# Performance work log

Measured on AMD Instinct MI355X. Metric: run time of the kernel, lower is better.

The kernel has to match this reference:

```python
import jax, jax.numpy as jnp
import numpy as np

TAU_MEM = 20.0
TAU_SYN = 5.0
ALPHA_MEM = float(np.exp(-1.0 / TAU_MEM))
ALPHA_SYN = float(np.exp(-1.0 / TAU_SYN))
CONNECTIVITY = 0.1
SPECTRAL_RADIUS = 0.9


def setup_inputs() -> dict:
    key = jax.random.key(0)
    k1, k2, k3, k4 = jax.random.split(key, 4)
    B, D, N = 2048, 256, 512
    rates = jax.random.normal(k1, (B, D), dtype=jnp.float32)
    input_weight = jax.random.normal(k2, (N, D), dtype=jnp.float32) * 0.1
    W = jax.random.normal(k3, (N, N), dtype=jnp.float32)
    mask = (jax.random.uniform(k4, (N, N)) < CONNECTIVITY).astype(jnp.float32)
    W = W * mask
    # mirror torch init: scale by spectral_radius / max eigvalsh
    max_eig = jnp.linalg.eigvalsh(W)[-1]
    W = W * (SPECTRAL_RADIUS / max_eig)
    return {
        "rates": rates,
        "input_weight": input_weight,
        "reservoir_weight": W,
        "v_mem": jnp.zeros((B, N), dtype=jnp.float32),
        "current": jnp.zeros((B, N), dtype=jnp.float32),
        "n_steps": 64,
    }


def reference(rates, input_weight, reservoir_weight, v_mem, current, n_steps):
    dtype = rates.dtype
    # input current is identical every step in the original loop -> hoist it
    input_current = rates @ input_weight.T  # (B, N)

    def step(carry, _):
        v, c, spike_sum = carry
        rec = (c > 0).astype(dtype) @ reservoir_weight  # (B, N)
        c = ALPHA_SYN * c + (1.0 - ALPHA_SYN) * (input_current + rec)
        v = ALPHA_MEM * v + (1.0 - ALPHA_MEM) * c
        spike_sum = spike_sum + (v > 0).astype(dtype)
        return (v, c, spike_sum), None

    (v, c, spike_sum), _ = jax.lax.scan(
        step, (v_mem, current, jnp.zeros_like(v_mem)), None, length=n_steps
    )
    readout = spike_sum / n_steps  # == stack(spikes).mean(dim=1)
    return readout, (v, c)
```

## Files before the change

kernel.cpp:

```cpp
#include <hip/hip_runtime.h>
#include <stdint.h>


#define N_NEU 512
#define B_ROWS 2048
#define D_IN 256
#define R_PB 8
#define NBLK (B_ROWS / R_PB)

#define WS_PERM    0
#define WS_RANK    2048
#define WS_CNT     4096
#define WS_CNTW    8192
#define WS_IBASE   8256
#define WS_WBASE   8320
#define WS_IDX     16384
#define WS_WT      81920

#define SPK_OFF(k)  ((k) << 4)
#define SPK_BUF     8192

#define H16_ONE 0x3C00u

__global__ __launch_bounds__(256) void lsm_count(
    const float* __restrict__ W, uint32_t* __restrict__ ws)
{
    int t  = threadIdx.x;
    int k0 = blockIdx.x * 4;
    int c0 = 0, c1 = 0;
    #pragma unroll
    for (int kk = 0; kk < 4; ++kk) {
        const float* row = W + (size_t)(k0 + kk) * N_NEU;
        c0 += (row[t]       != 0.0f) ? 1 : 0;
        c1 += (row[t + 256] != 0.0f) ? 1 : 0;
    }
    if (c0) atomicAdd(&ws[(WS_CNT >> 2) + t],       (uint32_t)c0);
    if (c1) atomicAdd(&ws[(WS_CNT >> 2) + t + 256], (uint32_t)c1);
}

__global__ __launch_bounds__(512) void lsm_sort(uint32_t* __restrict__ ws)
{
    __shared__ int hist[N_NEU + 1];
    __shared__ int csort[N_NEU];
    __shared__ int gcw[8];

    int t = threadIdx.x;
    int creal = (int)ws[(WS_CNT >> 2) + t];
    for (int i = t; i < N_NEU + 1; i += 512) hist[i] = 0;
    __syncthreads();
    atomicAdd(&hist[creal], 1);
    __syncthreads();
    if (t == 0) {
        int acc = 0;
        for (int v = 0; v <= N_NEU; ++v) { int h = hist[v]; hist[v] = acc; acc += h; }
    }
    __syncthreads();
    int rank = atomicAdd(&hist[creal], 1);
    ws[(WS_PERM >> 2) + rank] = (uint32_t)t;
    ws[(WS_RANK >> 2) + t]    = (uint32_t)rank;
    csort[rank] = creal;
    __syncthreads();
    if (t < 8) {
        int cw = csort[t * 64 + 63];
        cw = (cw + 7) & ~7;
        gcw[t] = cw;
        ws[(WS_CNTW >> 2) + t] = (uint32_t)cw;
    }
    __syncthreads();
    if (t == 0) {
        int ai = 0, aw = 0;
        for (int g = 0; g < 8; ++g) {
            ws[(WS_IBASE >> 2) + g] = (uint32_t)ai;
            ws[(WS_WBASE >> 2) + g] = (uint32_t)aw;
            ai += gcw[g] * 64 * 2;
            aw += gcw[g] * 64 * 4;
        }
    }
    __syncthreads();
    int wg = rank >> 6, ls = rank & 63;
    int cw = gcw[wg];
    uint32_t ib = ws[(WS_IBASE >> 2) + wg];
    uint32_t wb = ws[(WS_WBASE >> 2) + wg];
    char* base = (char*)ws;
    for (int j = creal; j < cw; ++j) {
        *(unsigned short*)(base + WS_IDX + ib + (j >> 3) * 1024 + ls * 16 + (j & 7) * 2) = 0;
        *(float*)(base + WS_WT + wb + (j >> 3) * 2048 + ls * 32 + (j & 7) * 4) = 0.0f;
    }
}

__global__ __launch_bounds__(64) void lsm_fill(
    const float* __restrict__ W, uint32_t* __restrict__ ws)
{
    int c    = blockIdx.x;
    int lane = threadIdx.x;
    char* base = (char*)ws;
    uint32_t rank = ws[(WS_RANK >> 2) + c];
    int wg = (int)(rank >> 6), ls = (int)(rank & 63);
    uint32_t ib = ws[(WS_IBASE >> 2) + wg];
    uint32_t wb = ws[(WS_WBASE >> 2) + wg];
    int rot = ls & 7;

    __shared__ int bcnt[8];
    __shared__ int bcur[8];
    if (lane < 8) bcnt[lane] = 0;
    __syncthreads();

    for (int k = lane; k < N_NEU; k += 64) {
        float wv = W[(size_t)k * N_NEU + c];
        if (wv != 0.0f) {
            int r = ((k & 7) - rot) & 7;
            atomicAdd(&bcnt[r], 1);
        }
    }
    __syncthreads();
    if (lane == 0) {
        int acc = 0;
        for (int r = 0; r < 8; ++r) { bcur[r] = acc; acc += bcnt[r]; }
    }
    __syncthreads();

    for (int k = lane; k < N_NEU; k += 64) {
        float wv = W[(size_t)k * N_NEU + c];
        if (wv != 0.0f) {
            int r = ((k & 7) - rot) & 7;
            int j = atomicAdd(&bcur[r], 1);
            *(unsigned short*)(base + WS_IDX + ib + (j >> 3) * 1024 + ls * 16 + (j & 7) * 2)
                = (unsigned short)SPK_OFF(k);
            *(float*)(base + WS_WT + wb + (j >> 3) * 2048 + ls * 32 + (j & 7) * 4) = wv;
        }
    }
}

#define GATH(P, X, B) \
    P##0 = *(const uint4*)((B) + ((X).x & 0xffffu)); \
    P##1 = *(const uint4*)((B) + ((X).x >> 16));     \
    P##2 = *(const uint4*)((B) + ((X).y & 0xffffu)); \
    P##3 = *(const uint4*)((B) + ((X).y >> 16));     \
    P##4 = *(const uint4*)((B) + ((X).z & 0xffffu)); \
    P##5 = *(const uint4*)((B) + ((X).z >> 16));     \
    P##6 = *(const uint4*)((B) + ((X).w & 0xffffu)); \
    P##7 = *(const uint4*)((B) + ((X).w >> 16));

#define FMIX_LO(ACC, WV, S) \
    asm("v_fma_mix_f32 %0, %1, %2, %0 op_sel:[0,0,0] op_sel_hi:[0,1,0]" \
        : "+v"(ACC) : "v"(WV), "v"(S));
#define FMIX_HI(ACC, WV, S) \
    asm("v_fma_mix_f32 %0, %1, %2, %0 op_sel:[0,1,0] op_sel_hi:[0,1,0]" \
        : "+v"(ACC) : "v"(WV), "v"(S));

#define C1(S, WV) \
    FMIX_LO(rec0, WV, (S).x) FMIX_HI(rec1, WV, (S).x) \
    FMIX_LO(rec2, WV, (S).y) FMIX_HI(rec3, WV, (S).y) \
    FMIX_LO(rec4, WV, (S).z) FMIX_HI(rec5, WV, (S).z) \
    FMIX_LO(rec6, WV, (S).w) FMIX_HI(rec7, WV, (S).w)

#define CONS(P, WA, WB) \
    C1(P##0, (WA).x) C1(P##1, (WA).y) C1(P##2, (WA).z) C1(P##3, (WA).w) \
    C1(P##4, (WB).x) C1(P##5, (WB).y) C1(P##6, (WB).z) C1(P##7, (WB).w)

#define LDW(WA, WB, K) \
    WA = ((const float4*)(wp0 + (K) * 2048))[0]; \
    WB = ((const float4*)(wp0 + (K) * 2048))[1];

__global__ __launch_bounds__(512, 1)
void lsm_main(
    const float* __restrict__ rates, const float* __restrict__ inW,
    const float* __restrict__ vin,   const float* __restrict__ cin,
    const int* __restrict__ nsteps_p,
    const uint32_t* __restrict__ ws, float* __restrict__ out)
{
    __shared__ __align__(16) unsigned char smem[2 * SPK_BUF + 16384];
    float* stg = (float*)(smem + 2 * SPK_BUF);
    float* rl  = stg;

    int q    = threadIdx.x;
    int blk  = blockIdx.x;
    int r0   = blk * R_PB;
    int w    = q >> 6;
    int lane = q & 63;
    int wg   = (w < 4) ? w : (11 - w);
    int n    = (int)ws[(WS_PERM >> 2) + wg * 64 + lane];
    int cw   = (int)ws[(WS_CNTW >> 2) + wg];
    int nit  = cw >> 3;
    const char* ip0 = (const char*)ws + WS_IDX + ws[(WS_IBASE >> 2) + wg]
                    + lane * 16;
    const char* wp0 = (const char*)ws + WS_WT  + ws[(WS_WBASE >> 2) + wg]
                    + lane * 32;
    int spk_n = SPK_OFF(n);

    float c0v[R_PB], v0v[R_PB];
    #pragma unroll
    for (int r = 0; r < R_PB; ++r)
        stg[r * N_NEU + q] = cin[(size_t)(r0 + r) * N_NEU + q];
    __syncthreads();
    #pragma unroll
    for (int r = 0; r < R_PB; ++r) c0v[r] = stg[r * N_NEU + n];
    __syncthreads();
    #pragma unroll
    for (int r = 0; r < R_PB; ++r)
        stg[r * N_NEU + q] = vin[(size_t)(r0 + r) * N_NEU + q];
    __syncthreads();
    #pragma unroll
    for (int r = 0; r < R_PB; ++r) v0v[r] = stg[r * N_NEU + n];
    __syncthreads();

    ((float4*)rl)[q] = ((const float4*)(rates + (size_t)r0 * D_IN))[q];
    __syncthreads();

    float I[R_PB] = {0.f, 0.f, 0.f, 0.f, 0.f, 0.f, 0.f, 0.f};
    {
        const float4* wrow = (const float4*)(inW + (size_t)n * D_IN);
        for (int d4 = 0; d4 < D_IN / 4; ++d4) {
            float4 wv = wrow[d4];
            #pragma unroll
            for (int r = 0; r < R_PB; ++r) {
                const float* rr = rl + r * D_IN + d4 * 4;
                I[r] += wv.x * rr[0] + wv.y * rr[1] + wv.z * rr[2] + wv.w * rr[3];
            }
        }
    }

    uint4 sini = make_uint4(0u, 0u, 0u, 0u);
    #pragma unroll
    for (int r = 0; r < R_PB; ++r) {
        unsigned hb = (c0v[r] > 0.f) ? H16_ONE : 0u;
        unsigned sh = (r & 1) ? 16 : 0;
        if (r < 2)      sini.x |= hb << sh;
        else if (r < 4) sini.y |= hb << sh;
        else if (r < 6) sini.z |= hb << sh;
        else            sini.w |= hb << sh;
    }
    *(uint4*)(smem + spk_n) = sini;

    unsigned ssx = 0u, ssy = 0u;

    uint4 xr0, xr1, xr2, xr3, xr4, xr5, xr6, xr7, xr8, xr9, xr10, xr11;
    const uint4 xz = make_uint4(0u, 0u, 0u, 0u);
    xr0  =              *(const uint4*)(ip0);
    xr1  = (1  < nit) ? *(const uint4*)(ip0 + 1024)  : xz;
    xr2  = (2  < nit) ? *(const uint4*)(ip0 + 2048)  : xz;
    xr3  = (3  < nit) ? *(const uint4*)(ip0 + 3072)  : xz;
    xr4  = (4  < nit) ? *(const uint4*)(ip0 + 4096)  : xz;
    xr5  = (5  < nit) ? *(const uint4*)(ip0 + 5120)  : xz;
    xr6  = (6  < nit) ? *(const uint4*)(ip0 + 6144)  : xz;
    xr7  = (7  < nit) ? *(const uint4*)(ip0 + 7168)  : xz;
    xr8  = (8  < nit) ? *(const uint4*)(ip0 + 8192)  : xz;
    xr9  = (9  < nit) ? *(const uint4*)(ip0 + 9216)  : xz;
    xr10 = (10 < nit) ? *(const uint4*)(ip0 + 10240) : xz;
    xr11 = (11 < nit) ? *(const uint4*)(ip0 + 11264) : xz;

    const float AS   = (float)0.8187307530779818;
    const float OMAS = (float)(1.0 - 0.8187307530779818);
    const float AM   = (float)0.9512294245007140;
    const float OMAM = (float)(1.0 - 0.9512294245007140);

    int T = nsteps_p[0];
    __syncthreads();

    #pragma unroll 1
    for (int t = 0; t < T; ++t) {
        const unsigned char* sb = smem + ((t & 1) ? SPK_BUF : 0);
        unsigned char*       db = smem + ((t & 1) ? 0 : SPK_BUF);

        float rec0 = 0.f, rec1 = 0.f, rec2 = 0.f, rec3 = 0.f;
        float rec4 = 0.f, rec5 = 0.f, rec6 = 0.f, rec7 = 0.f;
        uint4 a0, a1, a2, a3, a4, a5, a6, a7;
        uint4 b0, b1, b2, b3, b4, b5, b6, b7;
        float4 waA, wbA, waB, wbB;

        LDW(waA, wbA, 0)
        GATH(a, xr0, sb)
        if (1 < nit)  { LDW(waB, wbB, 1)  GATH(b, xr1, sb)  }
        CONS(a, waA, wbA)
        if (1 < nit)  {
            if (2 < nit)  { LDW(waA, wbA, 2)  GATH(a, xr2, sb)  }
            CONS(b, waB, wbB)
        }
        if (2 < nit)  {
            if (3 < nit)  { LDW(waB, wbB, 3)  GATH(b, xr3, sb)  }
            CONS(a, waA, wbA)
        }
        if (3 < nit)  {
            if (4 < nit)  { LDW(waA, wbA, 4)  GATH(a, xr4, sb)  }
            CONS(b, waB, wbB)
        }
        if (4 < nit)  {
            if (5 < nit)  { LDW(waB, wbB, 5)  GATH(b, xr5, sb)  }
            CONS(a, waA, wbA)
        }
        if (5 < nit)  {
            if (6 < nit)  { LDW(waA, wbA, 6)  GATH(a, xr6, sb)  }
            CONS(b, waB, wbB)
        }
        if (6 < nit)  {
            if (7 < nit)  { LDW(waB, wbB, 7)  GATH(b, xr7, sb)  }
            CONS(a, waA, wbA)
        }
        if (7 < nit)  {
            if (8 < nit)  { LDW(waA, wbA, 8)  GATH(a, xr8, sb)  }
            CONS(b, waB, wbB)
        }
        if (8 < nit)  {
            if (9 < nit)  { LDW(waB, wbB, 9)  GATH(b, xr9, sb)  }
            CONS(a, waA, wbA)
        }
        if (9 < nit)  {
            if (10 < nit) { LDW(waA, wbA, 10) GATH(a, xr10, sb) }
            CONS(b, waB, wbB)
        }
        if (10 < nit) {
            if (11 < nit) { LDW(waB, wbB, 11) GATH(b, xr11, sb) }
            CONS(a, waA, wbA)
        }
        if (11 < nit) {
            CONS(b, waB, wbB)
        }

        uint4 ns = make_uint4(0u, 0u, 0u, 0u);
        unsigned vbx = 0u, vby = 0u;
        {
            float rca[R_PB] = {rec0, rec1, rec2, rec3, rec4, rec5, rec6, rec7};
            #pragma unroll
            for (int r = 0; r < R_PB; ++r) {
                c0v[r] = AS * c0v[r] + OMAS * (I[r] + rca[r]);
                v0v[r] = AM * v0v[r] + OMAM * c0v[r];
                unsigned hb = (c0v[r] > 0.f) ? H16_ONE : 0u;
                unsigned vb = (v0v[r] > 0.f) ? 1u : 0u;
                unsigned sh = (r & 1) ? 16 : 0;
                if (r < 2)      ns.x |= hb << sh;
                else if (r < 4) ns.y |= hb << sh;
                else if (r < 6) ns.z |= hb << sh;
                else            ns.w |= hb << sh;
                if (r < 4) vbx |= vb << (r * 8);
                else       vby |= vb << ((r - 4) * 8);
            }
        }
        ssx += vbx;
        ssy += vby;
        *(uint4*)(db + spk_n) = ns;
        __syncthreads();
    }

    float invT = 1.0f / (float)T;
    size_t BN = (size_t)B_ROWS * N_NEU;

    #pragma unroll
    for (int r = 0; r < R_PB; ++r) {
        unsigned cnt = (r < 4) ? ((ssx >> (r * 8)) & 0xffu)
                               : ((ssy >> ((r - 4) * 8)) & 0xffu);
        stg[r * N_NEU + n] = (float)cnt * invT;
    }
    __syncthreads();
    #pragma unroll
    for (int r = 0; r < R_PB; ++r)
        out[(size_t)(r0 + r) * N_NEU + q] = stg[r * N_NEU + q];
    __syncthreads();

    #pragma unroll
    for (int r = 0; r < R_PB; ++r) stg[r * N_NEU + n] = v0v[r];
    __syncthreads();
    #pragma unroll
    for (int r = 0; r < R_PB; ++r)
        out[BN + (size_t)(r0 + r) * N_NEU + q] = stg[r * N_NEU + q];
    __syncthreads();

    #pragma unroll
    for (int r = 0; r < R_PB; ++r) stg[r * N_NEU + n] = c0v[r];
    __syncthreads();
    #pragma unroll
    for (int r = 0; r < R_PB; ++r)
        out[2 * BN + (size_t)(r0 + r) * N_NEU + q] = stg[r * N_NEU + q];
}

extern "C" void kernel_launch(void* const* d_in, const int* in_sizes, int n_in,
                              void* d_out, int out_size, void* d_ws, size_t ws_size,
                              hipStream_t stream)
{
    const float* rates = (const float*)d_in[0];
    const float* inW   = (const float*)d_in[1];
    const float* W     = (const float*)d_in[2];
    const float* vin   = (const float*)d_in[3];
    const float* cin   = (const float*)d_in[4];
    const int*   nst   = (const int*)d_in[5];
    uint32_t* ws = (uint32_t*)d_ws;
    float* out = (float*)d_out;
    (void)in_sizes; (void)n_in; (void)out_size; (void)ws_size;

    hipMemsetAsync((char*)d_ws + WS_CNT, 0, 2048, stream);

    lsm_count<<<128, 256, 0, stream>>>(W, ws);
    lsm_sort<<<1, 512, 0, stream>>>(ws);
    lsm_fill<<<N_NEU, 64, 0, stream>>>(W, ws);
    lsm_main<<<NBLK, 512, 0, stream>>>(rates, inW, vin, cin, nst, ws, out);
}
```

Before: 327.3 us.

## Fuse sparse-weight preprocessing and main loop into one cooperative kernel

Replaces the memset plus three preprocessing kernels (count, sort, fill) and the main kernel with a single cooperative launch that uses grid-wide syncs between phases. Each of the 256 blocks handles two rows or columns of the reservoir matrix during counting and filling, and block 0 does the sort. The goal is to remove several kernel launch gaps. In exchange it adds four grid barriers and requires all 256 blocks to be co-resident. The extra shared memory might also affect occupancy or whether the launch succeeds.

```diff
diff --git a/kernel.cpp b/kernel.cpp
--- a/kernel.cpp
+++ b/kernel.cpp
@@ -1,5 +1,8 @@
 #include <hip/hip_runtime.h>
+#include <hip/hip_cooperative_groups.h>
 #include <stdint.h>
+
+namespace cg = cooperative_groups;
 
 
 #define N_NEU 512
@@ -21,115 +24,6 @@
 #define SPK_BUF     8192
 
 #define H16_ONE 0x3C00u
-
-__global__ __launch_bounds__(256) void lsm_count(
-    const float* __restrict__ W, uint32_t* __restrict__ ws)
-{
-    int t  = threadIdx.x;
-    int k0 = blockIdx.x * 4;
-    int c0 = 0, c1 = 0;
-    #pragma unroll
-    for (int kk = 0; kk < 4; ++kk) {
-        const float* row = W + (size_t)(k0 + kk) * N_NEU;
-        c0 += (row[t]       != 0.0f) ? 1 : 0;
-        c1 += (row[t + 256] != 0.0f) ? 1 : 0;
-    }
-    if (c0) atomicAdd(&ws[(WS_CNT >> 2) + t],       (uint32_t)c0);
-    if (c1) atomicAdd(&ws[(WS_CNT >> 2) + t + 256], (uint32_t)c1);
-}
-
-__global__ __launch_bounds__(512) void lsm_sort(uint32_t* __restrict__ ws)
-{
-    __shared__ int hist[N_NEU + 1];
-    __shared__ int csort[N_NEU];
-    __shared__ int gcw[8];
-
-    int t = threadIdx.x;
-    int creal = (int)ws[(WS_CNT >> 2) + t];
-    for (int i = t; i < N_NEU + 1; i += 512) hist[i] = 0;
-    __syncthreads();
-    atomicAdd(&hist[creal], 1);
-    __syncthreads();
-    if (t == 0) {
-        int acc = 0;
-        for (int v = 0; v <= N_NEU; ++v) { int h = hist[v]; hist[v] = acc; acc += h; }
-    }
-    __syncthreads();
-    int rank = atomicAdd(&hist[creal], 1);
-    ws[(WS_PERM >> 2) + rank] = (uint32_t)t;
-    ws[(WS_RANK >> 2) + t]    = (uint32_t)rank;
-    csort[rank] = creal;
-    __syncthreads();
-    if (t < 8) {
-        int cw = csort[t * 64 + 63];
-        cw = (cw + 7) & ~7;
-        gcw[t] = cw;
-        ws[(WS_CNTW >> 2) + t] = (uint32_t)cw;
-    }
-    __syncthreads();
-    if (t == 0) {
-        int ai = 0, aw = 0;
-        for (int g = 0; g < 8; ++g) {
-            ws[(WS_IBASE >> 2) + g] = (uint32_t)ai;
-            ws[(WS_WBASE >> 2) + g] = (uint32_t)aw;
-            ai += gcw[g] * 64 * 2;
-            aw += gcw[g] * 64 * 4;
-        }
-    }
-    __syncthreads();
-    int wg = rank >> 6, ls = rank & 63;
-    int cw = gcw[wg];
-    uint32_t ib = ws[(WS_IBASE >> 2) + wg];
-    uint32_t wb = ws[(WS_WBASE >> 2) + wg];
-    char* base = (char*)ws;
-    for (int j = creal; j < cw; ++j) {
-        *(unsigned short*)(base + WS_IDX + ib + (j >> 3) * 1024 + ls * 16 + (j & 7) * 2) = 0;
-        *(float*)(base + WS_WT + wb + (j >> 3) * 2048 + ls * 32 + (j & 7) * 4) = 0.0f;
-    }
-}
-
-__global__ __launch_bounds__(64) void lsm_fill(
-    const float* __restrict__ W, uint32_t* __restrict__ ws)
-{
-    int c    = blockIdx.x;
-    int lane = threadIdx.x;
-    char* base = (char*)ws;
-    uint32_t rank = ws[(WS_RANK >> 2) + c];
-    int wg = (int)(rank >> 6), ls = (int)(rank & 63);
-    uint32_t ib = ws[(WS_IBASE >> 2) + wg];
-    uint32_t wb = ws[(WS_WBASE >> 2) + wg];
-    int rot = ls & 7;
-
-    __shared__ int bcnt[8];
-    __shared__ int bcur[8];
-    if (lane < 8) bcnt[lane] = 0;
-    __syncthreads();
-
-    for (int k = lane; k < N_NEU; k += 64) {
-        float wv = W[(size_t)k * N_NEU + c];
-        if (wv != 0.0f) {
-            int r = ((k & 7) - rot) & 7;
-            atomicAdd(&bcnt[r], 1);
-        }
-    }
-    __syncthreads();
-    if (lane == 0) {
-        int acc = 0;
-        for (int r = 0; r < 8; ++r) { bcur[r] = acc; acc += bcnt[r]; }
-    }
-    __syncthreads();
-
-    for (int k = lane; k < N_NEU; k += 64) {
-        float wv = W[(size_t)k * N_NEU + c];
-        if (wv != 0.0f) {
-            int r = ((k & 7) - rot) & 7;
-            int j = atomicAdd(&bcur[r], 1);
-            *(unsigned short*)(base + WS_IDX + ib + (j >> 3) * 1024 + ls * 16 + (j & 7) * 2)
-                = (unsigned short)SPK_OFF(k);
-            *(float*)(base + WS_WT + wb + (j >> 3) * 2048 + ls * 32 + (j & 7) * 4) = wv;
-        }
-    }
-}
 
 #define GATH(P, X, B) \
     P##0 = *(const uint4*)((B) + ((X).x & 0xffffu)); \
@@ -163,18 +57,129 @@
     WB = ((const float4*)(wp0 + (K) * 2048))[1];
 
 __global__ __launch_bounds__(512, 1)
-void lsm_main(
+void lsm_all(
     const float* __restrict__ rates, const float* __restrict__ inW,
+    const float* __restrict__ W,
     const float* __restrict__ vin,   const float* __restrict__ cin,
     const int* __restrict__ nsteps_p,
-    const uint32_t* __restrict__ ws, float* __restrict__ out)
+    uint32_t* __restrict__ ws, float* __restrict__ out)
 {
+    cg::grid_group grid = cg::this_grid();
+
     __shared__ __align__(16) unsigned char smem[2 * SPK_BUF + 16384];
+    __shared__ int hist[N_NEU + 1];
+    __shared__ int csort[N_NEU];
+    __shared__ int gcw8[8];
+    __shared__ int fcnt[2][8];
+    __shared__ int fcur[2][8];
+
     float* stg = (float*)(smem + 2 * SPK_BUF);
     float* rl  = stg;
 
-    int q    = threadIdx.x;
-    int blk  = blockIdx.x;
+    int q   = threadIdx.x;
+    int blk = blockIdx.x;
+
+    if (blk == 0) ws[(WS_CNT >> 2) + q] = 0u;
+    grid.sync();
+
+    {
+        const float* rA = W + (size_t)(2 * blk)     * N_NEU;
+        const float* rB = W + (size_t)(2 * blk + 1) * N_NEU;
+        int cc = ((rA[q] != 0.f) ? 1 : 0) + ((rB[q] != 0.f) ? 1 : 0);
+        if (cc) atomicAdd(&ws[(WS_CNT >> 2) + q], (uint32_t)cc);
+    }
+    grid.sync();
+
+    if (blk == 0) {
+        int t = q;
+        int creal = (int)ws[(WS_CNT >> 2) + t];
+        for (int i = t; i < N_NEU + 1; i += 512) hist[i] = 0;
+        __syncthreads();
+        atomicAdd(&hist[creal], 1);
+        __syncthreads();
+        if (t == 0) {
+            int acc = 0;
+            for (int v = 0; v <= N_NEU; ++v) { int h = hist[v]; hist[v] = acc; acc += h; }
+        }
+        __syncthreads();
+        int rank = atomicAdd(&hist[creal], 1);
+        ws[(WS_PERM >> 2) + rank] = (uint32_t)t;
+        ws[(WS_RANK >> 2) + t]    = (uint32_t)rank;
+        csort[rank] = creal;
+        __syncthreads();
+        if (t < 8) {
+            int cw2 = csort[t * 64 + 63];
+            cw2 = (cw2 + 7) & ~7;
+            gcw8[t] = cw2;
+            ws[(WS_CNTW >> 2) + t] = (uint32_t)cw2;
+        }
+        __syncthreads();
+        if (t == 0) {
+            int ai = 0, aw = 0;
+            for (int g = 0; g < 8; ++g) {
+                ws[(WS_IBASE >> 2) + g] = (uint32_t)ai;
+                ws[(WS_WBASE >> 2) + g] = (uint32_t)aw;
+                ai += gcw8[g] * 64 * 2;
+                aw += gcw8[g] * 64 * 4;
+            }
+        }
+        __syncthreads();
+        int wg2 = rank >> 6, ls2 = rank & 63;
+        int cw2 = gcw8[wg2];
+        uint32_t ib = ws[(WS_IBASE >> 2) + wg2];
+        uint32_t wb = ws[(WS_WBASE >> 2) + wg2];
+        char* base = (char*)ws;
+        for (int j = creal; j < cw2; ++j) {
+            *(unsigned short*)(base + WS_IDX + ib + (j >> 3) * 1024 + ls2 * 16 + (j & 7) * 2) = 0;
+            *(float*)(base + WS_WT + wb + (j >> 3) * 2048 + ls2 * 32 + (j & 7) * 4) = 0.0f;
+        }
+    }
+    grid.sync();
+
+    {
+        int wv = q >> 6, ln = q & 63;
+        if (q < 16) fcnt[q >> 3][q & 7] = 0;
+        __syncthreads();
+        if (wv < 2) {
+            int c = 2 * blk + wv;
+            uint32_t rank = ws[(WS_RANK >> 2) + c];
+            int rot = (int)(rank & 7u);
+            for (int k = ln; k < N_NEU; k += 64) {
+                float wvv = W[(size_t)k * N_NEU + c];
+                if (wvv != 0.f) {
+                    int r = ((k & 7) - rot) & 7;
+                    atomicAdd(&fcnt[wv][r], 1);
+                }
+            }
+        }
+        __syncthreads();
+        if (q < 2) {
+            int acc = 0;
+            for (int r = 0; r < 8; ++r) { fcur[q][r] = acc; acc += fcnt[q][r]; }
+        }
+        __syncthreads();
+        if (wv < 2) {
+            int c = 2 * blk + wv;
+            uint32_t rank = ws[(WS_RANK >> 2) + c];
+            int wg2 = (int)(rank >> 6), ls2 = (int)(rank & 63);
+            int rot = (int)(rank & 7u);
+            uint32_t ib = ws[(WS_IBASE >> 2) + wg2];
+            uint32_t wb = ws[(WS_WBASE >> 2) + wg2];
+            char* base = (char*)ws;
+            for (int k = ln; k < N_NEU; k += 64) {
+                float wvv = W[(size_t)k * N_NEU + c];
+                if (wvv != 0.f) {
+                    int r = ((k & 7) - rot) & 7;
+                    int j = atomicAdd(&fcur[wv][r], 1);
+                    *(unsigned short*)(base + WS_IDX + ib + (j >> 3) * 1024 + ls2 * 16 + (j & 7) * 2)
+                        = (unsigned short)SPK_OFF(k);
+                    *(float*)(base + WS_WT + wb + (j >> 3) * 2048 + ls2 * 32 + (j & 7) * 4) = wvv;
+                }
+            }
+        }
+    }
+    grid.sync();
+
     int r0   = blk * R_PB;
     int w    = q >> 6;
     int lane = q & 63;
@@ -211,11 +216,11 @@
     {
         const float4* wrow = (const float4*)(inW + (size_t)n * D_IN);
         for (int d4 = 0; d4 < D_IN / 4; ++d4) {
-            float4 wv = wrow[d4];
+            float4 wv2 = wrow[d4];
             #pragma unroll
             for (int r = 0; r < R_PB; ++r) {
                 const float* rr = rl + r * D_IN + d4 * 4;
-                I[r] += wv.x * rr[0] + wv.y * rr[1] + wv.z * rr[2] + wv.w * rr[3];
+                I[r] += wv2.x * rr[0] + wv2.y * rr[1] + wv2.z * rr[2] + wv2.w * rr[3];
             }
         }
     }
@@ -386,10 +391,10 @@
     float* out = (float*)d_out;
     (void)in_sizes; (void)n_in; (void)out_size; (void)ws_size;
 
-    hipMemsetAsync((char*)d_ws + WS_CNT, 0, 2048, stream);
-
-    lsm_count<<<128, 256, 0, stream>>>(W, ws);
-    lsm_sort<<<1, 512, 0, stream>>>(ws);
-    lsm_fill<<<N_NEU, 64, 0, stream>>>(W, ws);
-    lsm_main<<<NBLK, 512, 0, stream>>>(rates, inW, vin, cin, nst, ws, out);
+    void* kargs[] = {
+        (void*)&rates, (void*)&inW, (void*)&W, (void*)&vin, (void*)&cin,
+        (void*)&nst, (void*)&ws, (void*)&out
+    };
+    hipLaunchCooperativeKernel((const void*)lsm_all, dim3(NBLK), dim3(512),
+                               kargs, 0, stream);
 }
```

After: 428.9 us. 1.31x slower.
